# Performance work log

Measured on AMD Instinct MI355X. Metric: run time of the kernel, lower is better.

Reference implementation:

```python
import jax, jax.numpy as jnp
import numpy as np

HEADS = 4

def setup_inputs() -> dict:
    key = jax.random.key(0)
    ks = jax.random.split(key, 9)
    dim = 256
    s = 0.05  # small weight scale keeps softmax logits in a sane range
    x = jax.random.normal(ks[0], (4, dim, 48, 48), dtype=jnp.float32)
    wk = jax.random.normal(ks[1], (dim, dim), dtype=jnp.float32) * s
    bk = jax.random.normal(ks[2], (dim,), dtype=jnp.float32) * s
    wq = jax.random.normal(ks[3], (dim, dim), dtype=jnp.float32) * s
    bq = jax.random.normal(ks[4], (dim,), dtype=jnp.float32) * s
    wv = jax.random.normal(ks[5], (dim, dim), dtype=jnp.float32) * s
    bv = jax.random.normal(ks[6], (dim,), dtype=jnp.float32) * s
    wo = jax.random.normal(ks[7], (dim, dim), dtype=jnp.float32) * s
    bo = jax.random.normal(ks[8], (dim,), dtype=jnp.float32) * s
    return {"x": x, "wk": wk, "bk": bk, "wq": wq, "bq": bq,
            "wv": wv, "bv": bv, "wo": wo, "bo": bo}

def reference(x, wk, bk, wq, bq, wv, bv, wo, bo):
    b, C, h, w = x.shape
    hc = C // HEADS          # head_channels = dim // heads
    N = h * w

    def proj(W, bias):
        # Conv2d with 1x1 kernel == channel-mixing GEMM; reshape to [b, heads, hc, N]
        y = jnp.einsum('oc,bchw->bohw', W, x) + bias[None, :, None, None]
        return y.reshape(b, HEADS, hc, N)

    k = proj(wk, bk)
    q = proj(wq, bq)
    v = proj(wv, bv)

    # dots = k^T @ q : [b, heads, N_key, N_query]  (NOTE: original never applies self.scale)
    dots = jnp.einsum('bhcn,bhcm->bhnm', k, q)
    # softmax over dim=-2 (key axis) -> normalized over keys for each query column
    attn = jax.nn.softmax(dots, axis=-2)
    # out = v @ attn : [b, heads, hc, N_query]
    out = jnp.einsum('bhcn,bhnm->bhcm', v, attn).reshape(b, C, h, w)
    # unifyheads conv1x1 (dropout p=0 -> identity)
    return jnp.einsum('oc,bchw->bohw', wo, out) + bo[None, :, None, None]
```

## Files before the change

### kernel.cpp

```cpp
#include <hip/hip_runtime.h>
#include <math.h>

#define NB 4
#define CH 256
#define NHEADS 4
#define HC 64
#define NT 2304
#define NSEGS 4
#define KSEG 576
#define NSEG 9
#define NQT 18

typedef _Float16 f16;
typedef _Float16 f16x4 __attribute__((ext_vector_type(4)));
typedef _Float16 f16x8 __attribute__((ext_vector_type(8)));
typedef float f32x4 __attribute__((ext_vector_type(4)));
typedef float f32x16 __attribute__((ext_vector_type(16)));

#define MFMA16(a, b, c) __builtin_amdgcn_mfma_f32_16x16x32_f16(a, b, c, 0, 0, 0)
#define MFMA32(a, b, c) __builtin_amdgcn_mfma_f32_32x32x16_f16(a, b, c, 0, 0, 0)

__device__ __forceinline__ void gload_lds16(const void* g, void* l) {
    __builtin_amdgcn_global_load_lds(
        (const __attribute__((address_space(1))) unsigned int*)g,
        (__attribute__((address_space(3))) unsigned int*)l, 16, 0, 0);
}

__device__ __forceinline__ unsigned pkh(float a, float b) {
    auto r = __builtin_amdgcn_cvt_pkrtz(a, b);
    return __builtin_bit_cast(unsigned, r);
}
__device__ __forceinline__ void swap32(unsigned& a, unsigned& b) {
    asm volatile("v_permlane32_swap_b32 %0, %1" : "+v"(a), "+v"(b));
}

__global__ __launch_bounds__(256) void wcvt(
    const float* __restrict__ w0, const float* __restrict__ w1,
    const float* __restrict__ w2, const float* __restrict__ w3,
    f16* __restrict__ O)
{
    const int id = blockIdx.x * 256 + threadIdx.x;
    const int tsel = id >> 13;
    const int off = (id & 8191) * 8;
    const float* src = tsel == 0 ? w0 : (tsel == 1 ? w1 : (tsel == 2 ? w2 : w3));
    const float4 a = *reinterpret_cast<const float4*>(src + off);
    const float4 b = *reinterpret_cast<const float4*>(src + off + 4);
    f16x8 o = {(f16)a.x, (f16)a.y, (f16)a.z, (f16)a.w,
               (f16)b.x, (f16)b.y, (f16)b.z, (f16)b.w};
    *reinterpret_cast<f16x8*>(&O[(size_t)tsel * 65536 + off]) = o;
}

__global__ __launch_bounds__(256) void proj_qkv_v3(
    const f16* __restrict__ W16,
    const float* __restrict__ bk, const float* __restrict__ bq,
    const float* __restrict__ bv,
    const float* __restrict__ X,
    f16* __restrict__ Kt, f16* __restrict__ Qt, f16* __restrict__ Vg)
{
    __shared__ __align__(16) char SMEM[40960];
    f16 (*T)[264]  = reinterpret_cast<f16(*)[264]>(SMEM);
    f16 (*Vt)[80]  = reinterpret_cast<f16(*)[80]>(SMEM);

    const int t = threadIdx.x, l = t & 63, w = t >> 6;
    const int lm = l & 15, lg = l >> 4;
    const int n0 = blockIdx.x * 64;
    const int sel = blockIdx.y;
    const int b = blockIdx.z;

    const f16* W = W16 + (size_t)sel * 65536;
    const float* Bi = sel == 0 ? bk : (sel == 1 ? bq : bv);

    {
        const int cq = t >> 4;
        const int nq = (t & 15) * 4;
#pragma unroll
        for (int p = 0; p < 16; ++p) {
            const int c = p * 16 + cq;
            const float4 v = *reinterpret_cast<const float4*>(
                &X[((size_t)b * CH + c) * NT + n0 + nq]);
            T[nq + 0][c] = (f16)v.x;
            T[nq + 1][c] = (f16)v.y;
            T[nq + 2][c] = (f16)v.z;
            T[nq + 3][c] = (f16)v.w;
        }
    }
    __syncthreads();

    f32x4 acc[4][4] = {};

#pragma unroll 2
    for (int ks = 0; ks < 8; ++ks) {
        f16x8 bf[4];
#pragma unroll
        for (int nt = 0; nt < 4; ++nt)
            bf[nt] = *reinterpret_cast<const f16x8*>(
                &T[nt * 16 + lm][ks * 32 + lg * 8]);
#pragma unroll
        for (int h = 0; h < 4; ++h) {
            const f16x8 a = *reinterpret_cast<const f16x8*>(
                &W[(size_t)(h * 64 + w * 16 + lm) * CH + ks * 32 + lg * 8]);
#pragma unroll
            for (int nt = 0; nt < 4; ++nt)
                acc[h][nt] = MFMA16(a, bf[nt], acc[h][nt]);
        }
    }

    const int c_base = w * 16 + lg * 4;
    if (sel < 2) {
        f16* Out = sel == 0 ? Kt : Qt;
#pragma unroll
        for (int h = 0; h < 4; ++h) {
            const float4 b4 = *reinterpret_cast<const float4*>(&Bi[h * 64 + c_base]);
            const float bb[4] = {b4.x, b4.y, b4.z, b4.w};
#pragma unroll
            for (int nt = 0; nt < 4; ++nt) {
                const int n = n0 + nt * 16 + lm;
                f16x4 o = {(f16)(acc[h][nt][0] + bb[0]), (f16)(acc[h][nt][1] + bb[1]),
                           (f16)(acc[h][nt][2] + bb[2]), (f16)(acc[h][nt][3] + bb[3])};
                *reinterpret_cast<f16x4*>(
                    &Out[((size_t)((b * NHEADS + h) * NT + n)) * HC + c_base]) = o;
            }
        }
    } else {
        __syncthreads();
#pragma unroll
        for (int h = 0; h < 4; ++h)
#pragma unroll
            for (int nt = 0; nt < 4; ++nt)
#pragma unroll
                for (int r = 0; r < 4; ++r)
                    Vt[h * 64 + c_base + r][nt * 16 + lm] = (f16)acc[h][nt][r];
        __syncthreads();
#pragma unroll
        for (int p = 0; p < 8; ++p) {
            const int c  = p * 32 + (t >> 3);
            const int nn = (t & 7) * 8;
            const float bb = Bi[c];
            const f16x8 vv = *reinterpret_cast<const f16x8*>(&Vt[c][nn]);
            f16x8 o;
#pragma unroll
            for (int j = 0; j < 8; ++j) o[j] = (f16)((float)vv[j] + bb);
            *reinterpret_cast<f16x8*>(
                &Vg[((size_t)((b * NHEADS + (c >> 6)) * HC + (c & 63))) * NT
                    + n0 + nn]) = o;
        }
    }
}

__global__ __launch_bounds__(256) void attn_p1(
    const f16* __restrict__ Kt, const f16* __restrict__ Qt,
    const f16* __restrict__ Vg,
    f16* __restrict__ Pa, float* __restrict__ Pm, float* __restrict__ Pl)
{
    __shared__ f16 SM[2][4096];

    const int t = threadIdx.x, l = t & 63, w = t >> 6;
    const int col = l & 31, hi = l >> 5;

    const int bid = blockIdx.x;
    const int xcd = bid & 7, idx = bid >> 3;
    const int second = idx >= 72 ? 1 : 0;
    const int bh = 2 * xcd + second;
    const int idx2 = idx - 72 * second;
    const int qt = idx2 >> 2, seg = idx2 & 3;
    const int b = bh >> 2, h = bh & 3;
    const int m0 = qt * 128;

    const size_t bhs = (size_t)(b * NHEADS + h);
    const f16* Kb = Kt + bhs * NT * HC;
    const f16* Qb = Qt + bhs * NT * HC;
    const f16* Vb = Vg + bhs * HC * NT;

    const int srow = l >> 3, su = l & 7, sx = su ^ srow;

    const int q = m0 + w * 32 + col;
    f16x8 qf[4];
#pragma unroll
    for (int cs = 0; cs < 4; ++cs)
        qf[cs] = *reinterpret_cast<const f16x8*>(
            &Qb[(size_t)q * HC + cs * 16 + hi * 8]);

    const f32x16 Z16 = {0,0,0,0,0,0,0,0,0,0,0,0,0,0,0,0};
    f32x16 acc0 = Z16, acc1 = Z16;
    float m_run = -3.0e38f, l_run = 0.0f;

    const int kbase = seg * KSEG;

    auto stage = [&](int kc) {
        const int half = (w & 1) * 32;
        if (w < 2) {
            const char* src = (const char*)(Kb + (size_t)kc * HC);
            char* dst = (char*)&SM[0][0];
#pragma unroll
            for (int g = 0; g < 4; ++g) {
                const int rb = half + g * 8;
                gload_lds16(src + (size_t)(rb + srow) * 128 + (sx << 4),
                            dst + rb * 128);
            }
        } else {
            const char* src = (const char*)Vb + (size_t)kc * 2;
            char* dst = (char*)&SM[1][0];
#pragma unroll
            for (int g = 0; g < 4; ++g) {
                const int rb = half + g * 8;
                gload_lds16(src + (size_t)(rb + srow) * (NT * 2) + (sx << 4),
                            dst + rb * 128);
            }
        }
    };

    auto rd = [&](const f16* base, int row, int u) -> f16x8 {
        return *reinterpret_cast<const f16x8*>(
            base + row * 64 + ((u ^ (row & 7)) << 3));
    };

    stage(kbase);
    __syncthreads();

    for (int i = 0; i < NSEG; ++i) {
        const f16* Kc = &SM[0][0];
        const f16* Vc = &SM[1][0];

        f32x16 s0 = Z16, s1 = Z16;
#pragma unroll
        for (int cs = 0; cs < 4; ++cs) {
            const f16x8 k0 = rd(Kc, col,      cs * 2 + hi);
            const f16x8 k1 = rd(Kc, 32 + col, cs * 2 + hi);
            s0 = MFMA32(k0, qf[cs], s0);
            s1 = MFMA32(k1, qf[cs], s1);
        }

        float m8[8];
#pragma unroll
        for (int j = 0; j < 8; ++j)
            m8[j] = fmaxf(fmaxf(s0[2 * j], s0[2 * j + 1]),
                          fmaxf(s1[2 * j], s1[2 * j + 1]));
        float cm = fmaxf(fmaxf(fmaxf(m8[0], m8[1]), fmaxf(m8[2], m8[3])),
                         fmaxf(fmaxf(m8[4], m8[5]), fmaxf(m8[6], m8[7])));
        cm = fmaxf(cm, __shfl_xor(cm, 32));
        if (!__all(cm <= m_run + 8.0f)) {
            const float mN = fmaxf(m_run, cm);
            const float fac = __expf(m_run - mN);
#pragma unroll
            for (int r = 0; r < 16; ++r) { acc0[r] *= fac; acc1[r] *= fac; }
            l_run *= fac;
            m_run = mN;
        }
        float p0[16], p1[16];
        float ps0 = 0.f, ps1 = 0.f, ps2 = 0.f, ps3 = 0.f;
#pragma unroll
        for (int r = 0; r < 4; ++r) {
            p0[r]      = __expf(s0[r]      - m_run); ps0 += p0[r];
            p0[r + 4]  = __expf(s0[r + 4]  - m_run); ps1 += p0[r + 4];
            p0[r + 8]  = __expf(s0[r + 8]  - m_run); ps2 += p0[r + 8];
            p0[r + 12] = __expf(s0[r + 12] - m_run); ps3 += p0[r + 12];
            p1[r]      = __expf(s1[r]      - m_run); ps0 += p1[r];
            p1[r + 4]  = __expf(s1[r + 4]  - m_run); ps1 += p1[r + 4];
            p1[r + 8]  = __expf(s1[r + 8]  - m_run); ps2 += p1[r + 8];
            p1[r + 12] = __expf(s1[r + 12] - m_run); ps3 += p1[r + 12];
        }
        l_run += (ps0 + ps1) + (ps2 + ps3);

        unsigned a0[8], a1[8];
#pragma unroll
        for (int j = 0; j < 8; ++j) {
            a0[j] = pkh(p0[2 * j], p0[2 * j + 1]);
            a1[j] = pkh(p1[2 * j], p1[2 * j + 1]);
        }
        swap32(a0[0], a0[2]); swap32(a0[1], a0[3]);
        swap32(a0[4], a0[6]); swap32(a0[5], a0[7]);
        swap32(a1[0], a1[2]); swap32(a1[1], a1[3]);
        swap32(a1[4], a1[6]); swap32(a1[5], a1[7]);
        union BU { unsigned u[4]; f16x8 v; };
        BU fr[4];
        fr[0].u[0] = a0[0]; fr[0].u[1] = a0[1]; fr[0].u[2] = a0[2]; fr[0].u[3] = a0[3];
        fr[1].u[0] = a0[4]; fr[1].u[1] = a0[5]; fr[1].u[2] = a0[6]; fr[1].u[3] = a0[7];
        fr[2].u[0] = a1[0]; fr[2].u[1] = a1[1]; fr[2].u[2] = a1[2]; fr[2].u[3] = a1[3];
        fr[3].u[0] = a1[4]; fr[3].u[1] = a1[5]; fr[3].u[2] = a1[6]; fr[3].u[3] = a1[7];

#pragma unroll
        for (int kk = 0; kk < 4; ++kk) {
            const f16x8 v0 = rd(Vc, col,      kk * 2 + hi);
            const f16x8 v1 = rd(Vc, 32 + col, kk * 2 + hi);
            acc0 = MFMA32(v0, fr[kk].v, acc0);
            acc1 = MFMA32(v1, fr[kk].v, acc1);
        }

        __syncthreads();
        if (i + 1 < NSEG) {
            stage(kbase + (i + 1) * 64);
            __syncthreads();
        }
    }

    const float l_full = l_run + __shfl_xor(l_run, 32);
    const float inv = 1.0f / l_full;
    const size_t pq = ((size_t)((seg * 16 + bh) * NQT + qt)) * 128 + w * 32 + col;
    if (hi == 0) { Pm[pq] = m_run; Pl[pq] = l_full; }
    f16* row = Pa + pq * 64;
#pragma unroll
    for (int rq = 0; rq < 4; ++rq) {
        const int c0 = rq * 8 + hi * 4;
        f16x4 o0 = {(f16)(acc0[rq * 4 + 0] * inv), (f16)(acc0[rq * 4 + 1] * inv),
                    (f16)(acc0[rq * 4 + 2] * inv), (f16)(acc0[rq * 4 + 3] * inv)};
        f16x4 o1 = {(f16)(acc1[rq * 4 + 0] * inv), (f16)(acc1[rq * 4 + 1] * inv),
                    (f16)(acc1[rq * 4 + 2] * inv), (f16)(acc1[rq * 4 + 3] * inv)};
        *reinterpret_cast<f16x4*>(row + c0) = o0;
        *reinterpret_cast<f16x4*>(row + 32 + c0) = o1;
    }
}

__global__ __launch_bounds__(256) void attn_mg(
    const f16* __restrict__ Pa, const float* __restrict__ Pm,
    const float* __restrict__ Pl, f16* __restrict__ Ot)
{
    const int t = threadIdx.x;
    const int qt = blockIdx.x, bh = blockIdx.y;
    const int b = bh >> 2, h = bh & 3;
    const int ql = t >> 1, c0 = (t & 1) * 32;

    size_t ix[NSEGS];
    float m[NSEGS], c[NSEGS];
    float M = -3.0e38f;
#pragma unroll
    for (int s = 0; s < NSEGS; ++s) {
        ix[s] = ((size_t)((s * 16 + bh) * NQT + qt)) * 128 + ql;
        m[s] = Pm[ix[s]];
        M = fmaxf(M, m[s]);
    }
    float csum = 0.f;
#pragma unroll
    for (int s = 0; s < NSEGS; ++s) {
        c[s] = __expf(m[s] - M) * Pl[ix[s]];
        csum += c[s];
    }
    const float inv = 1.0f / csum;

    f16* dst = &Ot[((size_t)(b * NT + qt * 128 + ql)) * CH + h * HC + c0];
#pragma unroll
    for (int j4 = 0; j4 < 4; ++j4) {
        float v[8] = {};
#pragma unroll
        for (int s = 0; s < NSEGS; ++s) {
            const f16x8 a = *reinterpret_cast<const f16x8*>(
                Pa + ix[s] * 64 + c0 + j4 * 8);
#pragma unroll
            for (int j = 0; j < 8; ++j) v[j] += c[s] * (float)a[j];
        }
        f16x8 o;
#pragma unroll
        for (int j = 0; j < 8; ++j) o[j] = (f16)(v[j] * inv);
        *reinterpret_cast<f16x8*>(dst + j4 * 8) = o;
    }
}

__global__ __launch_bounds__(256) void out_gemm_v2(
    const f16* __restrict__ wo16, const float* __restrict__ bo,
    const f16* __restrict__ Ot, float* __restrict__ Y)
{
    const int t = threadIdx.x, l = t & 63, w = t >> 6;
    const int lm = l & 15, lg = l >> 4;
    const int n0 = blockIdx.x * 64;
    const int o0 = blockIdx.y * 64;
    const int b = blockIdx.z;

    f32x4 acc[4] = {{0.f,0.f,0.f,0.f},{0.f,0.f,0.f,0.f},
                    {0.f,0.f,0.f,0.f},{0.f,0.f,0.f,0.f}};
    const int o_row = o0 + w * 16 + lm;

#pragma unroll
    for (int ks = 0; ks < 8; ++ks) {
        const f16x8 a = *reinterpret_cast<const f16x8*>(
            &wo16[(size_t)o_row * CH + ks * 32 + lg * 8]);
#pragma unroll
        for (int nt = 0; nt < 4; ++nt) {
            const f16x8 bf = *reinterpret_cast<const f16x8*>(
                &Ot[((size_t)(b * NT + n0 + nt * 16 + lm)) * CH + ks * 32 + lg * 8]);
            acc[nt] = MFMA16(a, bf, acc[nt]);
        }
    }

    const int ob = o0 + w * 16 + lg * 4;
    const float4 bias4 = *reinterpret_cast<const float4*>(&bo[ob]);
    const float bb[4] = {bias4.x, bias4.y, bias4.z, bias4.w};
#pragma unroll
    for (int nt = 0; nt < 4; ++nt) {
        const int n = n0 + nt * 16 + lm;
#pragma unroll
        for (int r = 0; r < 4; ++r)
            Y[((size_t)(b * CH + ob + r)) * NT + n] = acc[nt][r] + bb[r];
    }
}

extern "C" void kernel_launch(void* const* d_in, const int* in_sizes, int n_in,
                              void* d_out, int out_size, void* d_ws, size_t ws_size,
                              hipStream_t stream) {
    (void)in_sizes; (void)n_in; (void)out_size; (void)ws_size;
    const float* x  = (const float*)d_in[0];
    const float* wk = (const float*)d_in[1];
    const float* bk = (const float*)d_in[2];
    const float* wq = (const float*)d_in[3];
    const float* bq = (const float*)d_in[4];
    const float* wv = (const float*)d_in[5];
    const float* bv = (const float*)d_in[6];
    const float* wo = (const float*)d_in[7];
    const float* bo = (const float*)d_in[8];
    float* out = (float*)d_out;

    const size_t SZ = (size_t)NB * NT * CH;
    f16* Kt  = (f16*)d_ws;
    f16* Qt  = Kt + SZ;
    f16* Vg  = Qt + SZ;
    f16* Ot  = Vg + SZ;
    f16* W16 = Ot + SZ;
    f16* Pa  = W16 + 4 * 65536;
    float* Pm = (float*)(Pa + (size_t)NSEGS * 16 * NQT * 128 * 64);
    float* Pl = Pm + (size_t)NSEGS * 16 * NQT * 128;

    wcvt<<<dim3(128), 256, 0, stream>>>(wk, wq, wv, wo, W16);
    proj_qkv_v3<<<dim3(36, 3, 4), 256, 0, stream>>>(
        W16, bk, bq, bv, x, Kt, Qt, Vg);
    attn_p1<<<dim3(1152), 256, 0, stream>>>(Kt, Qt, Vg, Pa, Pm, Pl);
    attn_mg<<<dim3(18, 16), 256, 0, stream>>>(Pa, Pm, Pl, Ot);
    out_gemm_v2<<<dim3(36, 4, 4), 256, 0, stream>>>(
        W16 + 3 * 65536, bo, Ot, out);
}
```

Baseline: 97.70 us.

## Double-buffer K/V staging in attention and fuse split-merge into output GEMM

The attention kernel now uses two LDS buffers so the next K/V chunk is loaded asynchronously while the current one is computed, which removes one barrier per iteration. The split-K merge kernel and the output projection GEMM are fused: each block merges the four segment partials for 64 queries across all heads into an LDS tile, then multiplies by the full 256x256 output weight. This drops the Ot intermediate buffer and one kernel launch. In exchange the fused kernel launches only 144 blocks, each doing more serial work, which may leave the GPU underused.

```diff
diff --git a/kernel.cpp b/kernel.cpp
--- a/kernel.cpp
+++ b/kernel.cpp
@@ -152,7 +152,7 @@
     const f16* __restrict__ Vg,
     f16* __restrict__ Pa, float* __restrict__ Pm, float* __restrict__ Pl)
 {
-    __shared__ f16 SM[2][4096];
+    __shared__ f16 SM[2][2][4096];
 
     const int t = threadIdx.x, l = t & 63, w = t >> 6;
     const int col = l & 31, hi = l >> 5;
@@ -186,11 +186,11 @@
 
     const int kbase = seg * KSEG;
 
-    auto stage = [&](int kc) {
+    auto stage = [&](int kc, int buf) {
         const int half = (w & 1) * 32;
         if (w < 2) {
             const char* src = (const char*)(Kb + (size_t)kc * HC);
-            char* dst = (char*)&SM[0][0];
+            char* dst = (char*)&SM[buf][0][0];
 #pragma unroll
             for (int g = 0; g < 4; ++g) {
                 const int rb = half + g * 8;
@@ -199,7 +199,7 @@
             }
         } else {
             const char* src = (const char*)Vb + (size_t)kc * 2;
-            char* dst = (char*)&SM[1][0];
+            char* dst = (char*)&SM[buf][1][0];
 #pragma unroll
             for (int g = 0; g < 4; ++g) {
                 const int rb = half + g * 8;
@@ -214,12 +214,15 @@
             base + row * 64 + ((u ^ (row & 7)) << 3));
     };
 
-    stage(kbase);
+    stage(kbase, 0);
     __syncthreads();
 
     for (int i = 0; i < NSEG; ++i) {
-        const f16* Kc = &SM[0][0];
-        const f16* Vc = &SM[1][0];
+        const int cur = i & 1;
+        if (i + 1 < NSEG) stage(kbase + (i + 1) * 64, cur ^ 1);
+
+        const f16* Kc = &SM[cur][0][0];
+        const f16* Vc = &SM[cur][1][0];
 
         f32x16 s0 = Z16, s1 = Z16;
 #pragma unroll
@@ -287,10 +290,6 @@
         }
 
         __syncthreads();
-        if (i + 1 < NSEG) {
-            stage(kbase + (i + 1) * 64);
-            __syncthreads();
-        }
     }
 
     const float l_full = l_run + __shfl_xor(l_run, 32);
@@ -310,85 +309,95 @@
     }
 }
 
-__global__ __launch_bounds__(256) void attn_mg(
+__global__ __launch_bounds__(256) void out_fused(
+    const f16* __restrict__ wo16, const float* __restrict__ bo,
     const f16* __restrict__ Pa, const float* __restrict__ Pm,
-    const float* __restrict__ Pl, f16* __restrict__ Ot)
+    const float* __restrict__ Pl, float* __restrict__ Y)
 {
-    const int t = threadIdx.x;
-    const int qt = blockIdx.x, bh = blockIdx.y;
-    const int b = bh >> 2, h = bh & 3;
-    const int ql = t >> 1, c0 = (t & 1) * 32;
-
-    size_t ix[NSEGS];
-    float m[NSEGS], c[NSEGS];
-    float M = -3.0e38f;
-#pragma unroll
-    for (int s = 0; s < NSEGS; ++s) {
-        ix[s] = ((size_t)((s * 16 + bh) * NQT + qt)) * 128 + ql;
-        m[s] = Pm[ix[s]];
-        M = fmaxf(M, m[s]);
-    }
-    float csum = 0.f;
-#pragma unroll
-    for (int s = 0; s < NSEGS; ++s) {
-        c[s] = __expf(m[s] - M) * Pl[ix[s]];
-        csum += c[s];
-    }
-    const float inv = 1.0f / csum;
-
-    f16* dst = &Ot[((size_t)(b * NT + qt * 128 + ql)) * CH + h * HC + c0];
-#pragma unroll
-    for (int j4 = 0; j4 < 4; ++j4) {
-        float v[8] = {};
-#pragma unroll
-        for (int s = 0; s < NSEGS; ++s) {
-            const f16x8 a = *reinterpret_cast<const f16x8*>(
-                Pa + ix[s] * 64 + c0 + j4 * 8);
-#pragma unroll
-            for (int j = 0; j < 8; ++j) v[j] += c[s] * (float)a[j];
-        }
-        f16x8 o;
-#pragma unroll
-        for (int j = 0; j < 8; ++j) o[j] = (f16)(v[j] * inv);
-        *reinterpret_cast<f16x8*>(dst + j4 * 8) = o;
-    }
-}
-
-__global__ __launch_bounds__(256) void out_gemm_v2(
-    const f16* __restrict__ wo16, const float* __restrict__ bo,
-    const f16* __restrict__ Ot, float* __restrict__ Y)
-{
+    __shared__ f16 T[64][264];
+
     const int t = threadIdx.x, l = t & 63, w = t >> 6;
     const int lm = l & 15, lg = l >> 4;
     const int n0 = blockIdx.x * 64;
-    const int o0 = blockIdx.y * 64;
-    const int b = blockIdx.z;
-
-    f32x4 acc[4] = {{0.f,0.f,0.f,0.f},{0.f,0.f,0.f,0.f},
-                    {0.f,0.f,0.f,0.f},{0.f,0.f,0.f,0.f}};
-    const int o_row = o0 + w * 16 + lm;
-
-#pragma unroll
+    const int b = blockIdx.y;
+    const int qt = n0 >> 7, ql0 = n0 & 127;
+
+    {
+        const int n = t >> 2, c16 = (t & 3) * 16;
+#pragma unroll
+        for (int h = 0; h < 4; ++h) {
+            const int bh = b * NHEADS + h;
+            size_t ix[NSEGS];
+            float m[NSEGS], c[NSEGS];
+            float M = -3.0e38f;
+#pragma unroll
+            for (int s = 0; s < NSEGS; ++s) {
+                ix[s] = ((size_t)((s * 16 + bh) * NQT + qt)) * 128 + ql0 + n;
+                m[s] = Pm[ix[s]];
+                M = fmaxf(M, m[s]);
+            }
+            float csum = 0.f;
+#pragma unroll
+            for (int s = 0; s < NSEGS; ++s) {
+                c[s] = __expf(m[s] - M) * Pl[ix[s]];
+                csum += c[s];
+            }
+            const float inv = 1.0f / csum;
+            float v[16] = {};
+#pragma unroll
+            for (int s = 0; s < NSEGS; ++s) {
+                const f16* r = Pa + ix[s] * 64 + c16;
+                const f16x8 a0 = *reinterpret_cast<const f16x8*>(r);
+                const f16x8 a1 = *reinterpret_cast<const f16x8*>(r + 8);
+#pragma unroll
+                for (int j = 0; j < 8; ++j) {
+                    v[j]     += c[s] * (float)a0[j];
+                    v[8 + j] += c[s] * (float)a1[j];
+                }
+            }
+            f16x8 o0, o1;
+#pragma unroll
+            for (int j = 0; j < 8; ++j) {
+                o0[j] = (f16)(v[j] * inv);
+                o1[j] = (f16)(v[8 + j] * inv);
+            }
+            *reinterpret_cast<f16x8*>(&T[n][h * 64 + c16]) = o0;
+            *reinterpret_cast<f16x8*>(&T[n][h * 64 + c16 + 8]) = o1;
+        }
+    }
+    __syncthreads();
+
+    f32x4 acc[4][4] = {};
+#pragma unroll 2
     for (int ks = 0; ks < 8; ++ks) {
-        const f16x8 a = *reinterpret_cast<const f16x8*>(
-            &wo16[(size_t)o_row * CH + ks * 32 + lg * 8]);
+        f16x8 bf[4];
+#pragma unroll
+        for (int nt = 0; nt < 4; ++nt)
+            bf[nt] = *reinterpret_cast<const f16x8*>(
+                &T[nt * 16 + lm][ks * 32 + lg * 8]);
+#pragma unroll
+        for (int hp = 0; hp < 4; ++hp) {
+            const f16x8 a = *reinterpret_cast<const f16x8*>(
+                &wo16[(size_t)(hp * 64 + w * 16 + lm) * CH + ks * 32 + lg * 8]);
+#pragma unroll
+            for (int nt = 0; nt < 4; ++nt)
+                acc[hp][nt] = MFMA16(a, bf[nt], acc[hp][nt]);
+        }
+    }
+
+    const int c_base = w * 16 + lg * 4;
+#pragma unroll
+    for (int hp = 0; hp < 4; ++hp) {
+        const float4 b4 = *reinterpret_cast<const float4*>(&bo[hp * 64 + c_base]);
+        const float bb[4] = {b4.x, b4.y, b4.z, b4.w};
 #pragma unroll
         for (int nt = 0; nt < 4; ++nt) {
-            const f16x8 bf = *reinterpret_cast<const f16x8*>(
-                &Ot[((size_t)(b * NT + n0 + nt * 16 + lm)) * CH + ks * 32 + lg * 8]);
-            acc[nt] = MFMA16(a, bf, acc[nt]);
-        }
-    }
-
-    const int ob = o0 + w * 16 + lg * 4;
-    const float4 bias4 = *reinterpret_cast<const float4*>(&bo[ob]);
-    const float bb[4] = {bias4.x, bias4.y, bias4.z, bias4.w};
-#pragma unroll
-    for (int nt = 0; nt < 4; ++nt) {
-        const int n = n0 + nt * 16 + lm;
-#pragma unroll
-        for (int r = 0; r < 4; ++r)
-            Y[((size_t)(b * CH + ob + r)) * NT + n] = acc[nt][r] + bb[r];
+            const int n = n0 + nt * 16 + lm;
+#pragma unroll
+            for (int r = 0; r < 4; ++r)
+                Y[((size_t)(b * CH + hp * 64 + c_base + r)) * NT + n] =
+                    acc[hp][nt][r] + bb[r];
+        }
     }
 }
 
@@ -411,8 +420,7 @@
     f16* Kt  = (f16*)d_ws;
     f16* Qt  = Kt + SZ;
     f16* Vg  = Qt + SZ;
-    f16* Ot  = Vg + SZ;
-    f16* W16 = Ot + SZ;
+    f16* W16 = Vg + SZ;
     f16* Pa  = W16 + 4 * 65536;
     float* Pm = (float*)(Pa + (size_t)NSEGS * 16 * NQT * 128 * 64);
     float* Pl = Pm + (size_t)NSEGS * 16 * NQT * 128;
@@ -421,7 +429,6 @@
     proj_qkv_v3<<<dim3(36, 3, 4), 256, 0, stream>>>(
         W16, bk, bq, bv, x, Kt, Qt, Vg);
     attn_p1<<<dim3(1152), 256, 0, stream>>>(Kt, Qt, Vg, Pa, Pm, Pl);
-    attn_mg<<<dim3(18, 16), 256, 0, stream>>>(Pa, Pm, Pl, Ot);
-    out_gemm_v2<<<dim3(36, 4, 4), 256, 0, stream>>>(
-        W16 + 3 * 65536, bo, Ot, out);
-}
+    out_fused<<<dim3(36, 4), 256, 0, stream>>>(
+        W16 + 3 * 65536, bo, Pa, Pm, Pl, out);
+}
```

Result: faster. 86.36 us (-11.6%).
